# Kernel tuning notes

Measured on AMD Instinct MI355X. Metric: run time of the kernel, lower is better.

## Reference

```python
import jax, jax.numpy as jnp
import numpy as np

EPS = 1e-5

def bitlinear158(x, W):
    # BitNet b1.58 weight ternarization: beta = 1/mean(|W|), w_q = round(W*beta).clamp(-1,1)/beta
    beta = 1.0 / jnp.clip(jnp.mean(jnp.abs(W)), EPS, None)
    w_q = jnp.clip(jnp.round(W * beta), -1.0, 1.0) / beta
    # straight-through estimator (no-op in pure forward, kept for faithfulness)
    w = W + jax.lax.stop_gradient(w_q - W)
    return x @ w.T

def lrelu(x):
    return jnp.where(x >= 0, x, 0.2 * x)

def setup_inputs() -> dict:
    key = jax.random.key(0)
    ks = jax.random.split(key, 12)
    B, D_IN, H, L, Z = 65536, 784, 400, 200, 2
    def w(k, fan_out, fan_in):
        bound = 1.0 / np.sqrt(fan_in)
        return jax.random.uniform(k, (fan_out, fan_in), jnp.float32, -bound, bound)
    return {
        "x": jax.random.uniform(ks[0], (B, D_IN), jnp.float32),
        "epsilon": jax.random.normal(ks[1], (B, Z), jnp.float32),
        "W_e1": w(ks[2], H, D_IN),
        "W_e2": w(ks[3], H, H),
        "W_e3": w(ks[4], L, H),
        "W_mu": w(ks[5], Z, L),
        "W_lv": w(ks[6], Z, L),
        "W_d1": w(ks[7], L, Z),
        "W_d2": w(ks[8], H, L),
        "W_d3": w(ks[9], H, H),
        "W_d4": w(ks[10], H, H),
        "W_d5": w(ks[11], D_IN, H),
    }

def reference(x, epsilon, W_e1, W_e2, W_e3, W_mu, W_lv, W_d1, W_d2, W_d3, W_d4, W_d5):
    # encoder
    h = lrelu(bitlinear158(x, W_e1))
    h = lrelu(bitlinear158(h, W_e2))
    h = lrelu(bitlinear158(h, W_e3))
    mean = bitlinear158(h, W_mu)
    logvar = bitlinear158(h, W_lv)
    # reparameterization (source uses logvar directly as 'var')
    z = mean + logvar * epsilon
    # decoder
    d = lrelu(bitlinear158(z, W_d1))
    d = lrelu(bitlinear158(d, W_d2))
    d = lrelu(bitlinear158(d, W_d3))
    d = lrelu(bitlinear158(d, W_d4))
    x_hat = jax.nn.sigmoid(bitlinear158(d, W_d5))
    return (x_hat, mean, logvar)
```

## Files before the change

### kernel.cpp

```cpp
#include <hip/hip_runtime.h>

using u16 = unsigned short;
using u32 = unsigned int;

typedef __attribute__((ext_vector_type(8))) short bf16x8;
typedef __attribute__((ext_vector_type(4))) float f32x4;
typedef __attribute__((ext_vector_type(8))) u16 u16x8;

static __device__ __forceinline__ float b2f(u16 u) {
  return __uint_as_float((u32)u << 16);
}
static __device__ __forceinline__ u16 f2b(float f) {
  u32 x = __float_as_uint(f);
  return (u16)((x + 0x7fffu + ((x >> 16) & 1u)) >> 16);
}
static __device__ __forceinline__ void gload_lds16(const void* g, void* l) {
  __builtin_amdgcn_global_load_lds(
      (const __attribute__((address_space(1))) void*)g,
      (__attribute__((address_space(3))) void*)l, 16, 0, 0);
}

struct WMeta {
  const float* src;
  u16* dst;
  int N, K, Np, Kp, scaleIdx, blockStart;
};
struct PrepArgs { WMeta w[10]; };

__global__ __launch_bounds__(256)
void absmean_part(PrepArgs pa, double* __restrict__ partials)
{
  const int w = blockIdx.x >> 6;
  const int p = blockIdx.x & 63;
  const WMeta mw = pa.w[w];
  const long n = (long)mw.N * mw.K;
  const long chunk = (n + 63) >> 6;
  const long lo = (long)p * chunk;
  const long hi = min(n, lo + chunk);
  double sum = 0.0;
  for (long i = lo + threadIdx.x; i < hi; i += 256)
    sum += (double)fabsf(mw.src[i]);
  __shared__ double red[256];
  red[threadIdx.x] = sum;
  __syncthreads();
  for (int off = 128; off > 0; off >>= 1) {
    if (threadIdx.x < off) red[threadIdx.x] += red[threadIdx.x + off];
    __syncthreads();
  }
  if (threadIdx.x == 0) partials[blockIdx.x] = red[0];
}

__global__ __launch_bounds__(64)
void absmean_final(PrepArgs pa, const double* __restrict__ partials,
                   float* __restrict__ scales)
{
  const int w = threadIdx.x;
  if (w < 10) {
    double s = 0.0;
    #pragma unroll
    for (int i = 0; i < 64; ++i) s += partials[(w << 6) + i];
    const WMeta mw = pa.w[w];
    double m = s / (double)((long)mw.N * mw.K);
    scales[mw.scaleIdx] = (float)fmax(m, 1e-5);
  }
}

__global__ __launch_bounds__(256)
void ternarize_k(PrepArgs pa, const float* __restrict__ scales)
{
  const int b = blockIdx.x;
  int w = 0;
  #pragma unroll
  for (int i = 1; i < 10; ++i) if (b >= pa.w[i].blockStart) w = i;
  const WMeta mw = pa.w[w];
  const float inv = 1.0f / scales[mw.scaleIdx];
  const int tot = mw.Np * mw.Kp;
  int idx = (b - mw.blockStart) * 2048 + threadIdx.x * 8;
  #pragma unroll
  for (int j = 0; j < 8; ++j, ++idx) {
    if (idx < tot) {
      const int nn = idx / mw.Kp;
      const int kk = idx - nn * mw.Kp;
      float v = 0.f;
      if (nn < mw.N && kk < mw.K) {
        float t = rintf(mw.src[(size_t)nn * mw.K + kk] * inv);
        v = fminf(1.f, fmaxf(-1.f, t));
      }
      mw.dst[idx] = f2b(v);
    }
  }
}

__global__ __launch_bounds__(256)
void convert_x(const float* __restrict__ x, u16* __restrict__ xb)
{
  const int s = blockIdx.x * 256 + threadIdx.x;
  const int row = s / 104;
  const int c8 = s - row * 104;
  u16x8 o = (u16x8)(u16)0;
  if (c8 < 98) {
    const float4* px = (const float4*)(x + (size_t)row * 784 + c8 * 8);
    float4 v0 = px[0], v1 = px[1];
    o[0] = f2b(v0.x); o[1] = f2b(v0.y); o[2] = f2b(v0.z); o[3] = f2b(v0.w);
    o[4] = f2b(v1.x); o[5] = f2b(v1.y); o[6] = f2b(v1.z); o[7] = f2b(v1.w);
  }
  *(u16x8*)(xb + (size_t)row * 832 + c8 * 8) = o;
}

static __device__ __forceinline__ bf16x8 lds_frag(const u16* t, int row0, int lane, int kk) {
  int row = row0 + (lane & 15);
  int kb = (kk << 6) + ((lane >> 4) << 4);
  int off = row * 128 + (kb ^ ((row & 7) << 4));
  return *(const bf16x8*)((const char*)t + off);
}

template<bool LRELU, bool SIGMOID, bool OUTBF16>
__global__ __launch_bounds__(256)
void gemm_bt(const u16* __restrict__ A, const u16* __restrict__ Bw,
             void* __restrict__ Out, const float* __restrict__ sptr,
             int Kp, int ldOut, int Nstore)
{
  __shared__ __align__(16) u16 lsA[128 * 64];
  __shared__ __align__(16) u16 lsB[128 * 64];
  const int tid = threadIdx.x;
  const int lane = tid & 63, wid = tid >> 6;
  const int m0 = blockIdx.x << 7, n0 = blockIdx.y << 7;
  const int wr = wid >> 1, wc = wid & 1;
  f32x4 acc[4][4] = {};
  const int ksteps = Kp >> 6;
  for (int ks = 0; ks < ksteps; ++ks) {
    const size_t kbase = (size_t)ks << 6;
    #pragma unroll
    for (int it = 0; it < 4; ++it) {
      const int s = (it << 8) + tid;
      const int r = s >> 3;
      const int cc = (s & 7) ^ (r & 7);
      u16* dA = lsA + ((size_t)((it << 8) + (wid << 6)) << 3);
      u16* dB = lsB + ((size_t)((it << 8) + (wid << 6)) << 3);
      gload_lds16(A + (size_t)(m0 + r) * Kp + kbase + (cc << 3), dA);
      gload_lds16(Bw + (size_t)(n0 + r) * Kp + kbase + (cc << 3), dB);
    }
    __syncthreads();
    #pragma unroll
    for (int kk = 0; kk < 2; ++kk) {
      bf16x8 av[4], bv[4];
      #pragma unroll
      for (int m = 0; m < 4; ++m) av[m] = lds_frag(lsA, (wr << 6) + (m << 4), lane, kk);
      #pragma unroll
      for (int n = 0; n < 4; ++n) bv[n] = lds_frag(lsB, (wc << 6) + (n << 4), lane, kk);
      #pragma unroll
      for (int m = 0; m < 4; ++m)
        #pragma unroll
        for (int n = 0; n < 4; ++n)
          acc[m][n] = __builtin_amdgcn_mfma_f32_16x16x32_bf16(av[m], bv[n], acc[m][n], 0, 0, 0);
    }
    __syncthreads();
  }
  const float s = *sptr;
  const int colb = n0 + (wc << 6);
  const int rowb = m0 + (wr << 6);
  #pragma unroll
  for (int n = 0; n < 4; ++n) {
    const int col = colb + (n << 4) + (lane & 15);
    if (col >= Nstore) continue;
    #pragma unroll
    for (int m = 0; m < 4; ++m) {
      const int row0 = rowb + (m << 4) + ((lane >> 4) << 2);
      #pragma unroll
      for (int r = 0; r < 4; ++r) {
        float v = acc[m][n][r] * s;
        if (LRELU)   v = v >= 0.f ? v : 0.2f * v;
        if (SIGMOID) v = 1.f / (1.f + __expf(-v));
        if (OUTBF16) ((u16*)Out)[(size_t)(row0 + r) * ldOut + col] = f2b(v);
        else         ((float*)Out)[(size_t)(row0 + r) * ldOut + col] = v;
      }
    }
  }
}

__global__ __launch_bounds__(256)
void mid_kernel(const u16* __restrict__ h3, const u16* __restrict__ wmulv,
                const u16* __restrict__ wd1, const float* __restrict__ eps,
                float* __restrict__ outMean, float* __restrict__ outLv,
                u16* __restrict__ hd1, const float* __restrict__ scales)
{
  __shared__ __align__(16) u16 wML[1024];
  __shared__ u32 wD1s[256];
  __shared__ float zz[64][2];
  const int tid = threadIdx.x;
  if (tid < 128) ((u16x8*)wML)[tid] = ((const u16x8*)wmulv)[tid];
  wD1s[tid] = ((const u32*)wd1)[tid];
  __syncthreads();
  const float smu = scales[3], slv = scales[4], sd1 = scales[5];
  const int rl = tid >> 2, q = tid & 3;
  const size_t row = (size_t)blockIdx.x * 64 + rl;
  float a0 = 0.f, a1 = 0.f, a2 = 0.f, a3 = 0.f;
  const u16* hrow = h3 + row * 256 + q * 64;
  #pragma unroll
  for (int k8 = 0; k8 < 8; ++k8) {
    u16x8 hv = *(const u16x8*)(hrow + k8 * 8);
    u16x8 w0 = *(const u16x8*)(wML +   0 + q * 64 + k8 * 8);
    u16x8 w1 = *(const u16x8*)(wML + 256 + q * 64 + k8 * 8);
    u16x8 w2 = *(const u16x8*)(wML + 512 + q * 64 + k8 * 8);
    u16x8 w3 = *(const u16x8*)(wML + 768 + q * 64 + k8 * 8);
    #pragma unroll
    for (int j = 0; j < 8; ++j) {
      const float hf = b2f(hv[j]);
      a0 += hf * b2f(w0[j]);
      a1 += hf * b2f(w1[j]);
      a2 += hf * b2f(w2[j]);
      a3 += hf * b2f(w3[j]);
    }
  }
  a0 += __shfl_xor(a0, 1); a0 += __shfl_xor(a0, 2);
  a1 += __shfl_xor(a1, 1); a1 += __shfl_xor(a1, 2);
  a2 += __shfl_xor(a2, 1); a2 += __shfl_xor(a2, 2);
  a3 += __shfl_xor(a3, 1); a3 += __shfl_xor(a3, 2);
  if (q == 0) {
    const float m0v = a0 * smu, m1v = a1 * smu;
    const float l0v = a2 * slv, l1v = a3 * slv;
    const float e0 = eps[row * 2], e1 = eps[row * 2 + 1];
    outMean[row * 2]     = m0v; outMean[row * 2 + 1] = m1v;
    outLv[row * 2]       = l0v; outLv[row * 2 + 1]   = l1v;
    zz[rl][0] = m0v + l0v * e0;
    zz[rl][1] = m1v + l1v * e1;
  }
  __syncthreads();
  const u32 wp = wD1s[tid];
  const float t0 = b2f((u16)(wp & 0xffffu));
  const float t1 = b2f((u16)(wp >> 16));
  const bool live = tid < 200;
  u16* ocol = hd1 + ((size_t)blockIdx.x * 64) * 256 + tid;
  #pragma unroll 4
  for (int it = 0; it < 64; ++it) {
    float v = live ? sd1 * (zz[it][0] * t0 + zz[it][1] * t1) : 0.f;
    v = v >= 0.f ? v : 0.2f * v;
    ocol[(size_t)it * 256] = f2b(v);
  }
}

extern "C" void kernel_launch(void* const* d_in, const int* in_sizes, int n_in,
                              void* d_out, int out_size, void* d_ws, size_t ws_size,
                              hipStream_t stream)
{
  (void)in_sizes; (void)n_in; (void)out_size; (void)ws_size;
  const float* x   = (const float*)d_in[0];
  const float* eps = (const float*)d_in[1];
  float* out_f = (float*)d_out;

  float* scales = (float*)d_ws;
  u16* wb = (u16*)((char*)d_ws + 256);
  constexpr size_t E1 = 0;
  constexpr size_t E2 = 425984;
  constexpr size_t E3 = 655360;
  constexpr size_t MULV = 770048;
  constexpr size_t D1 = 771072;
  constexpr size_t D2 = 771584;
  constexpr size_t D3 = 902656;
  constexpr size_t D4 = 1132032;
  constexpr size_t D5 = 1361408;
  constexpr size_t WTOT = 1762816;
  u16* bufA = (u16*)((char*)d_ws + 256 + WTOT * 2);
  u16* bufB = (u16*)((char*)bufA + (size_t)65536 * 832 * 2);
  double* partials = (double*)bufA;

  PrepArgs pa;
  auto setw = [&](int i, int di, size_t off, int N, int K, int Np, int Kp, int bs) {
    pa.w[i] = WMeta{ (const float*)d_in[di], wb + off, N, K, Np, Kp, i, bs };
  };
  setw(0,  2, E1,        400, 784, 512, 832,   0);
  setw(1,  3, E2,        400, 400, 512, 448, 208);
  setw(2,  4, E3,        200, 400, 256, 448, 320);
  setw(3,  5, MULV,        2, 200,   2, 256, 376);
  setw(4,  6, MULV + 512,  2, 200,   2, 256, 377);
  setw(5,  7, D1,        200,   2, 256,   2, 378);
  setw(6,  8, D2,        400, 200, 512, 256, 379);
  setw(7,  9, D3,        400, 400, 512, 448, 443);
  setw(8, 10, D4,        400, 400, 512, 448, 555);
  setw(9, 11, D5,        784, 400, 896, 448, 667);

  absmean_part<<<640, 256, 0, stream>>>(pa, partials);
  absmean_final<<<1, 64, 0, stream>>>(pa, partials, scales);
  ternarize_k<<<863, 256, 0, stream>>>(pa, scales);
  convert_x<<<26624, 256, 0, stream>>>(x, bufA);

  dim3 blk(256);
  gemm_bt<true , false, true ><<<dim3(512, 4), blk, 0, stream>>>(bufA, wb + E1, bufB, scales + 0, 832, 448, 448);
  gemm_bt<true , false, true ><<<dim3(512, 4), blk, 0, stream>>>(bufB, wb + E2, bufA, scales + 1, 448, 448, 448);
  gemm_bt<true , false, true ><<<dim3(512, 2), blk, 0, stream>>>(bufA, wb + E3, bufB, scales + 2, 448, 256, 256);
  mid_kernel<<<1024, 256, 0, stream>>>(bufB, wb + MULV, wb + D1, eps,
                                       out_f + (size_t)65536 * 784,
                                       out_f + (size_t)65536 * 784 + 131072,
                                       bufA, scales);
  gemm_bt<true , false, true ><<<dim3(512, 4), blk, 0, stream>>>(bufA, wb + D2, bufB, scales + 6, 256, 448, 448);
  gemm_bt<true , false, true ><<<dim3(512, 4), blk, 0, stream>>>(bufB, wb + D3, bufA, scales + 7, 448, 448, 448);
  gemm_bt<true , false, true ><<<dim3(512, 4), blk, 0, stream>>>(bufA, wb + D4, bufB, scales + 8, 448, 448, 448);
  gemm_bt<false, true , false><<<dim3(512, 7), blk, 0, stream>>>(bufB, wb + D5, (void*)out_f, scales + 9, 448, 784, 784);
}
```

Measured before the change: 818.3 us.

## Replace 128x128 GEMM with 256x256-tile, triple-buffered LDS pipelined kernel

The bf16 MFMA GEMM moves from 128x128 tiles with 256 threads and a synchronous load/compute loop to 256x256 tiles with 512 threads, a 3-slot LDS ring buffer with two K-steps of prefetch, and explicit vmcnt waits with raised priority around the MFMA block. K padding grows to multiples of 32-element-aligned tiles (832->896, 448->512) and N padding to 256 multiples, so weight buffers, workspace offsets and convert_x strides are all relaid. The larger tile cuts global and LDS traffic per flop and overlaps loads with compute. In exchange it computes more padded work (for example 512 columns for 400, and 1024 for 784), uses 96KB of LDS and more registers per block, and halves the grid size, which lowers occupancy.

```diff
diff --git a/kernel.cpp b/kernel.cpp
--- a/kernel.cpp
+++ b/kernel.cpp
@@ -95,8 +95,8 @@
 void convert_x(const float* __restrict__ x, u16* __restrict__ xb)
 {
   const int s = blockIdx.x * 256 + threadIdx.x;
-  const int row = s / 104;
-  const int c8 = s - row * 104;
+  const int row = s / 112;
+  const int c8 = s - row * 112;
   u16x8 o = (u16x8)(u16)0;
   if (c8 < 98) {
     const float4* px = (const float4*)(x + (size_t)row * 784 + c8 * 8);
@@ -104,68 +104,92 @@
     o[0] = f2b(v0.x); o[1] = f2b(v0.y); o[2] = f2b(v0.z); o[3] = f2b(v0.w);
     o[4] = f2b(v1.x); o[5] = f2b(v1.y); o[6] = f2b(v1.z); o[7] = f2b(v1.w);
   }
-  *(u16x8*)(xb + (size_t)row * 832 + c8 * 8) = o;
-}
-
-static __device__ __forceinline__ bf16x8 lds_frag(const u16* t, int row0, int lane, int kk) {
-  int row = row0 + (lane & 15);
-  int kb = (kk << 6) + ((lane >> 4) << 4);
-  int off = row * 128 + (kb ^ ((row & 7) << 4));
-  return *(const bf16x8*)((const char*)t + off);
+  *(u16x8*)(xb + (size_t)row * 896 + c8 * 8) = o;
 }
 
 template<bool LRELU, bool SIGMOID, bool OUTBF16>
-__global__ __launch_bounds__(256)
-void gemm_bt(const u16* __restrict__ A, const u16* __restrict__ Bw,
+__global__ __launch_bounds__(512, 2)
+void gemm256(const u16* __restrict__ A, const u16* __restrict__ Bw,
              void* __restrict__ Out, const float* __restrict__ sptr,
              int Kp, int ldOut, int Nstore)
 {
-  __shared__ __align__(16) u16 lsA[128 * 64];
-  __shared__ __align__(16) u16 lsB[128 * 64];
+  __shared__ __align__(16) u16 lds[3 * 16384];
   const int tid = threadIdx.x;
   const int lane = tid & 63, wid = tid >> 6;
-  const int m0 = blockIdx.x << 7, n0 = blockIdx.y << 7;
-  const int wr = wid >> 1, wc = wid & 1;
-  f32x4 acc[4][4] = {};
-  const int ksteps = Kp >> 6;
-  for (int ks = 0; ks < ksteps; ++ks) {
-    const size_t kbase = (size_t)ks << 6;
-    #pragma unroll
-    for (int it = 0; it < 4; ++it) {
-      const int s = (it << 8) + tid;
-      const int r = s >> 3;
-      const int cc = (s & 7) ^ (r & 7);
-      u16* dA = lsA + ((size_t)((it << 8) + (wid << 6)) << 3);
-      u16* dB = lsB + ((size_t)((it << 8) + (wid << 6)) << 3);
-      gload_lds16(A + (size_t)(m0 + r) * Kp + kbase + (cc << 3), dA);
-      gload_lds16(Bw + (size_t)(n0 + r) * Kp + kbase + (cc << 3), dB);
+  const int wr = wid >> 2, wc = wid & 3;
+  const int m0 = blockIdx.x << 8, n0 = blockIdx.y << 8;
+  const int NT = Kp >> 5;
+
+  const int srow = tid >> 2;
+  const int sk = (((tid & 3) ^ ((tid >> 3) & 3)) << 3);
+  const size_t gA0 = (size_t)(m0 + srow) * Kp + sk;
+  const size_t gA1 = (size_t)(m0 + 128 + srow) * Kp + sk;
+  const size_t gB0 = (size_t)(n0 + srow) * Kp + sk;
+  const size_t gB1 = (size_t)(n0 + 128 + srow) * Kp + sk;
+  const int ldst = wid << 9;
+
+  auto stage = [&](int kt, int slot) {
+    u16* base = lds + slot * 16384;
+    const int ke = kt << 5;
+    gload_lds16(A + gA0 + ke, base + ldst);
+    gload_lds16(A + gA1 + ke, base + 4096 + ldst);
+    gload_lds16(Bw + gB0 + ke, base + 8192 + ldst);
+    gload_lds16(Bw + gB1 + ke, base + 12288 + ldst);
+  };
+
+  const int cs = (((lane >> 4) ^ ((lane >> 1) & 3)) << 4);
+  int offA[8], offB[4];
+  #pragma unroll
+  for (int m = 0; m < 8; ++m)
+    offA[m] = ((wr << 7) + (m << 4) + (lane & 15)) * 64 + cs;
+  #pragma unroll
+  for (int n = 0; n < 4; ++n)
+    offB[n] = ((wc << 6) + (n << 4) + (lane & 15)) * 64 + cs + 16384;
+
+  f32x4 acc[8][4] = {};
+  stage(0, 0);
+  stage(1, 1);
+  int slot = 0;
+  for (int kt = 0; kt < NT; ++kt) {
+    asm volatile("s_waitcnt lgkmcnt(0)" ::: "memory");
+    __builtin_amdgcn_s_barrier();
+    asm volatile("" ::: "memory");
+    int st2 = slot + 2; if (st2 >= 3) st2 -= 3;
+    if (kt + 2 < NT) {
+      stage(kt + 2, st2);
+      asm volatile("s_waitcnt vmcnt(8)" ::: "memory");
+    } else if (kt + 1 < NT) {
+      asm volatile("s_waitcnt vmcnt(4)" ::: "memory");
+    } else {
+      asm volatile("s_waitcnt vmcnt(0)" ::: "memory");
     }
-    __syncthreads();
-    #pragma unroll
-    for (int kk = 0; kk < 2; ++kk) {
-      bf16x8 av[4], bv[4];
+    __builtin_amdgcn_s_barrier();
+    asm volatile("" ::: "memory");
+
+    const char* lbase = (const char*)(lds + slot * 16384);
+    bf16x8 av[8], bv[4];
+    #pragma unroll
+    for (int m = 0; m < 8; ++m) av[m] = *(const bf16x8*)(lbase + offA[m]);
+    #pragma unroll
+    for (int n = 0; n < 4; ++n) bv[n] = *(const bf16x8*)(lbase + offB[n]);
+    __builtin_amdgcn_s_setprio(1);
+    #pragma unroll
+    for (int m = 0; m < 8; ++m)
       #pragma unroll
-      for (int m = 0; m < 4; ++m) av[m] = lds_frag(lsA, (wr << 6) + (m << 4), lane, kk);
-      #pragma unroll
-      for (int n = 0; n < 4; ++n) bv[n] = lds_frag(lsB, (wc << 6) + (n << 4), lane, kk);
-      #pragma unroll
-      for (int m = 0; m < 4; ++m)
-        #pragma unroll
-        for (int n = 0; n < 4; ++n)
-          acc[m][n] = __builtin_amdgcn_mfma_f32_16x16x32_bf16(av[m], bv[n], acc[m][n], 0, 0, 0);
-    }
-    __syncthreads();
-  }
+      for (int n = 0; n < 4; ++n)
+        acc[m][n] = __builtin_amdgcn_mfma_f32_16x16x32_bf16(av[m], bv[n], acc[m][n], 0, 0, 0);
+    __builtin_amdgcn_s_setprio(0);
+    slot = (slot == 2) ? 0 : slot + 1;
+  }
+
   const float s = *sptr;
-  const int colb = n0 + (wc << 6);
-  const int rowb = m0 + (wr << 6);
   #pragma unroll
   for (int n = 0; n < 4; ++n) {
-    const int col = colb + (n << 4) + (lane & 15);
+    const int col = n0 + (wc << 6) + (n << 4) + (lane & 15);
     if (col >= Nstore) continue;
     #pragma unroll
-    for (int m = 0; m < 4; ++m) {
-      const int row0 = rowb + (m << 4) + ((lane >> 4) << 2);
+    for (int m = 0; m < 8; ++m) {
+      const int row0 = m0 + (wr << 7) + (m << 4) + ((lane >> 4) << 2);
       #pragma unroll
       for (int r = 0; r < 4; ++r) {
         float v = acc[m][n][r] * s;
@@ -251,49 +275,49 @@
   float* scales = (float*)d_ws;
   u16* wb = (u16*)((char*)d_ws + 256);
   constexpr size_t E1 = 0;
-  constexpr size_t E2 = 425984;
-  constexpr size_t E3 = 655360;
-  constexpr size_t MULV = 770048;
-  constexpr size_t D1 = 771072;
-  constexpr size_t D2 = 771584;
-  constexpr size_t D3 = 902656;
-  constexpr size_t D4 = 1132032;
-  constexpr size_t D5 = 1361408;
-  constexpr size_t WTOT = 1762816;
+  constexpr size_t E2 = 458752;
+  constexpr size_t E3 = 720896;
+  constexpr size_t MULV = 851968;
+  constexpr size_t D1 = 852992;
+  constexpr size_t D2 = 853504;
+  constexpr size_t D3 = 984576;
+  constexpr size_t D4 = 1246720;
+  constexpr size_t D5 = 1508864;
+  constexpr size_t WTOT = 2033152;
   u16* bufA = (u16*)((char*)d_ws + 256 + WTOT * 2);
-  u16* bufB = (u16*)((char*)bufA + (size_t)65536 * 832 * 2);
+  u16* bufB = (u16*)((char*)bufA + (size_t)65536 * 896 * 2);
   double* partials = (double*)bufA;
 
   PrepArgs pa;
   auto setw = [&](int i, int di, size_t off, int N, int K, int Np, int Kp, int bs) {
     pa.w[i] = WMeta{ (const float*)d_in[di], wb + off, N, K, Np, Kp, i, bs };
   };
-  setw(0,  2, E1,        400, 784, 512, 832,   0);
-  setw(1,  3, E2,        400, 400, 512, 448, 208);
-  setw(2,  4, E3,        200, 400, 256, 448, 320);
-  setw(3,  5, MULV,        2, 200,   2, 256, 376);
-  setw(4,  6, MULV + 512,  2, 200,   2, 256, 377);
-  setw(5,  7, D1,        200,   2, 256,   2, 378);
-  setw(6,  8, D2,        400, 200, 512, 256, 379);
-  setw(7,  9, D3,        400, 400, 512, 448, 443);
-  setw(8, 10, D4,        400, 400, 512, 448, 555);
-  setw(9, 11, D5,        784, 400, 896, 448, 667);
+  setw(0,  2, E1,        400, 784, 512, 896,   0);
+  setw(1,  3, E2,        400, 400, 512, 512, 224);
+  setw(2,  4, E3,        200, 400, 256, 512, 352);
+  setw(3,  5, MULV,        2, 200,   2, 256, 416);
+  setw(4,  6, MULV + 512,  2, 200,   2, 256, 417);
+  setw(5,  7, D1,        200,   2, 256,   2, 418);
+  setw(6,  8, D2,        400, 200, 512, 256, 419);
+  setw(7,  9, D3,        400, 400, 512, 512, 483);
+  setw(8, 10, D4,        400, 400, 512, 512, 611);
+  setw(9, 11, D5,        784, 400,1024, 512, 739);
 
   absmean_part<<<640, 256, 0, stream>>>(pa, partials);
   absmean_final<<<1, 64, 0, stream>>>(pa, partials, scales);
-  ternarize_k<<<863, 256, 0, stream>>>(pa, scales);
-  convert_x<<<26624, 256, 0, stream>>>(x, bufA);
-
-  dim3 blk(256);
-  gemm_bt<true , false, true ><<<dim3(512, 4), blk, 0, stream>>>(bufA, wb + E1, bufB, scales + 0, 832, 448, 448);
-  gemm_bt<true , false, true ><<<dim3(512, 4), blk, 0, stream>>>(bufB, wb + E2, bufA, scales + 1, 448, 448, 448);
-  gemm_bt<true , false, true ><<<dim3(512, 2), blk, 0, stream>>>(bufA, wb + E3, bufB, scales + 2, 448, 256, 256);
+  ternarize_k<<<995, 256, 0, stream>>>(pa, scales);
+  convert_x<<<28672, 256, 0, stream>>>(x, bufA);
+
+  dim3 blk(512);
+  gemm256<true , false, true ><<<dim3(256, 2), blk, 0, stream>>>(bufA, wb + E1, bufB, scales + 0, 896, 512, 512);
+  gemm256<true , false, true ><<<dim3(256, 2), blk, 0, stream>>>(bufB, wb + E2, bufA, scales + 1, 512, 512, 512);
+  gemm256<true , false, true ><<<dim3(256, 1), blk, 0, stream>>>(bufA, wb + E3, bufB, scales + 2, 512, 256, 256);
   mid_kernel<<<1024, 256, 0, stream>>>(bufB, wb + MULV, wb + D1, eps,
                                        out_f + (size_t)65536 * 784,
                                        out_f + (size_t)65536 * 784 + 131072,
                                        bufA, scales);
-  gemm_bt<true , false, true ><<<dim3(512, 4), blk, 0, stream>>>(bufA, wb + D2, bufB, scales + 6, 256, 448, 448);
-  gemm_bt<true , false, true ><<<dim3(512, 4), blk, 0, stream>>>(bufB, wb + D3, bufA, scales + 7, 448, 448, 448);
-  gemm_bt<true , false, true ><<<dim3(512, 4), blk, 0, stream>>>(bufA, wb + D4, bufB, scales + 8, 448, 448, 448);
-  gemm_bt<false, true , false><<<dim3(512, 7), blk, 0, stream>>>(bufB, wb + D5, (void*)out_f, scales + 9, 448, 784, 784);
-}
+  gemm256<true , false, true ><<<dim3(256, 2), blk, 0, stream>>>(bufA, wb + D2, bufB, scales + 6, 256, 512, 512);
+  gemm256<true , false, true ><<<dim3(256, 2), blk, 0, stream>>>(bufB, wb + D3, bufA, scales + 7, 512, 512, 512);
+  gemm256<true , false, true ><<<dim3(256, 2), blk, 0, stream>>>(bufA, wb + D4, bufB, scales + 8, 512, 512, 512);
+  gemm256<false, true , false><<<dim3(256, 4), blk, 0, stream>>>(bufB, wb + D5, (void*)out_f, scales + 9, 512, 784, 784);
+}
```

Result: slower. 936.6 us (+14.5%).
